# Kernel optimization log

Measured on AMD Instinct MI355X. Metric: run time of the kernel, lower is better.

## Reference

```python
import jax, jax.numpy as jnp
import numpy as np

N_NODES = 50000
N_EDGES = 800000
F = 64
R = 32


def setup_inputs() -> dict:
    key = jax.random.key(0)
    ks = jax.random.split(key, 12)
    s = jax.random.normal(ks[0], (N_NODES, F), dtype=jnp.float32)
    v = jax.random.normal(ks[1], (N_NODES, 3, F), dtype=jnp.float32)
    radial_embeddings = jax.random.normal(ks[2], (N_EDGES, R), dtype=jnp.float32)
    f_cut = jax.random.uniform(ks[3], (N_EDGES,), dtype=jnp.float32)
    unit_vectors = jax.random.normal(ks[4], (N_EDGES, 3), dtype=jnp.float32)
    edge_index = jax.random.randint(ks[5], (2, N_EDGES), 0, N_NODES, dtype=jnp.int64 if jax.config.jax_enable_x64 else jnp.int32)
    # mlp_phi: Linear(F,F) -> SiLU -> Linear(F, 3F); linear_W: Linear(R, 3F)
    W1 = jax.random.normal(ks[6], (F, F), dtype=jnp.float32) / np.sqrt(F)
    b1 = jnp.zeros((F,), dtype=jnp.float32)
    W2 = jax.random.normal(ks[7], (F, 3 * F), dtype=jnp.float32) / np.sqrt(F)
    b2 = jnp.zeros((3 * F,), dtype=jnp.float32)
    Wr = jax.random.normal(ks[8], (R, 3 * F), dtype=jnp.float32) / np.sqrt(R)
    br = jnp.zeros((3 * F,), dtype=jnp.float32)
    return {"s": s, "v": v, "radial_embeddings": radial_embeddings, "f_cut": f_cut,
            "unit_vectors": unit_vectors, "edge_index": edge_index,
            "W1": W1, "b1": b1, "W2": W2, "b2": b2, "Wr": Wr, "br": br}


def reference(s, v, radial_embeddings, f_cut, unit_vectors, edge_index, W1, b1, W2, b2, Wr, br):
    idx_i, idx_j = edge_index[0], edge_index[1]
    n_nodes = s.shape[0]
    nf = s.shape[-1]
    # per-node MLP: Linear -> SiLU -> Linear to 3F channels
    phi = jax.nn.silu(s @ W1 + b1) @ W2 + b2            # [N, 3F]
    # radial filter weighted by cutoff
    W = (radial_embeddings @ Wr + br) * f_cut[:, None]   # [E, 3F]
    x = phi[idx_j] * W                                   # [E, 3F]  (gather + multiply)
    x_s, x_vv, x_vs = x[:, :nf], x[:, nf:2 * nf], x[:, 2 * nf:]
    ds = jax.ops.segment_sum(x_s, idx_i, num_segments=n_nodes)          # [N, F]
    x_v = v[idx_j] * x_vv[:, None, :] + x_vs[:, None, :] * unit_vectors[:, :, None]  # [E, 3, F]
    dv = jax.ops.segment_sum(x_v, idx_i, num_segments=n_nodes)          # [N, 3, F]
    return s + ds, v + dv
```

## Files before the change

### kernel.cpp

```cpp
#include <hip/hip_runtime.h>
#include <math.h>

#define N_NODES 50000
#define N_EDGES 800000
#define F 64
#define R 32
#define C3F 192
#define CAP 48
#define MLP_BLOCKS ((N_NODES + 31) / 32)
#define FILL_BLOCKS ((N_EDGES + 255) / 256)

#define REP32(X) X(0) X(1) X(2) X(3) X(4) X(5) X(6) X(7) \
                 X(8) X(9) X(10) X(11) X(12) X(13) X(14) X(15) \
                 X(16) X(17) X(18) X(19) X(20) X(21) X(22) X(23) \
                 X(24) X(25) X(26) X(27) X(28) X(29) X(30) X(31)

__global__ __launch_bounds__(256) void mlp_fill_kernel(
    const float* __restrict__ s, const float* __restrict__ W1,
    const float* __restrict__ b1, const float* __restrict__ W2,
    const float* __restrict__ b2, float* __restrict__ phi,
    const int* __restrict__ eidx, int* __restrict__ counts,
    int2* __restrict__ bucket)
{
    __shared__ float hid_s[32][68];

    if (blockIdx.x >= MLP_BLOCKS) {
        int e = (blockIdx.x - MLP_BLOCKS) * 256 + threadIdx.x;
        if (e < N_EDGES) {
            int i = eidx[e];
            int j = eidx[N_EDGES + e];
            int pos = atomicAdd(&counts[i], 1);
            if (pos < CAP) bucket[(size_t)i * CAP + pos] = make_int2(e, j);
        }
        return;
    }

    int n = threadIdx.x >> 3;
    int seg = threadIdx.x & 7;
    int node = blockIdx.x * 32 + n;
    bool live = node < N_NODES;

    if (live) {
        float sv[F];
        const float4* srow = (const float4*)(s + (size_t)node * F);
#pragma unroll
        for (int q = 0; q < F / 4; q++) {
            float4 t = srow[q];
            sv[4*q+0] = t.x; sv[4*q+1] = t.y; sv[4*q+2] = t.z; sv[4*q+3] = t.w;
        }
        float acc[8];
#pragma unroll
        for (int q = 0; q < 8; q++) acc[q] = b1[seg * 8 + q];
#pragma unroll
        for (int k = 0; k < F; k++) {
            float sk = sv[k];
            const float4* w = (const float4*)(W1 + (size_t)k * F + seg * 8);
            float4 w0 = w[0], w1 = w[1];
            acc[0] += sk * w0.x; acc[1] += sk * w0.y;
            acc[2] += sk * w0.z; acc[3] += sk * w0.w;
            acc[4] += sk * w1.x; acc[5] += sk * w1.y;
            acc[6] += sk * w1.z; acc[7] += sk * w1.w;
        }
#pragma unroll
        for (int q = 0; q < 8; q++) {
            float a = acc[q];
            hid_s[n][seg * 8 + q] = a / (1.f + __expf(-a));
        }
    }
    __syncthreads();

    if (!live) return;

    float hv[F];
#pragma unroll
    for (int q = 0; q < F; q++) hv[q] = hid_s[n][q];

    float acc[24];
#pragma unroll
    for (int q = 0; q < 24; q++) acc[q] = b2[seg * 24 + q];
#pragma unroll
    for (int k = 0; k < F; k++) {
        float hk = hv[k];
        const float4* w = (const float4*)(W2 + (size_t)k * C3F + seg * 24);
#pragma unroll
        for (int q4 = 0; q4 < 6; q4++) {
            float4 wv = w[q4];
            acc[q4*4+0] += hk * wv.x;
            acc[q4*4+1] += hk * wv.y;
            acc[q4*4+2] += hk * wv.z;
            acc[q4*4+3] += hk * wv.w;
        }
    }
    float4* o = (float4*)(phi + (size_t)node * C3F + seg * 24);
#pragma unroll
    for (int q4 = 0; q4 < 6; q4++)
        o[q4] = make_float4(acc[q4*4+0], acc[q4*4+1], acc[q4*4+2], acc[q4*4+3]);
}

__global__ __launch_bounds__(256, 3) void gather_kernel(
    const float* __restrict__ s, const float* __restrict__ v,
    const float* __restrict__ phi, const float* __restrict__ radial,
    const float* __restrict__ f_cut, const float* __restrict__ unit_vec,
    const float* __restrict__ Wr, const float* __restrict__ br,
    const int* __restrict__ counts, const int2* __restrict__ bucket,
    float* __restrict__ out_s, float* __restrict__ out_v)
{
    int lane = threadIdx.x & 63;
    int node = __builtin_amdgcn_readfirstlane(
        (int)blockIdx.x * 4 + (int)(threadIdx.x >> 6));
    if (node >= N_NODES) return;

#define DECL_WR(r) float wrs##r, wrv##r, wrq##r;
    REP32(DECL_WR)
#undef DECL_WR
#define LOAD_WR(r) { const float* w_ = Wr + (r) * C3F; \
                     wrs##r = w_[lane]; wrv##r = w_[64 + lane]; \
                     wrq##r = w_[128 + lane]; }
    REP32(LOAD_WR)
#undef LOAD_WR

    float b_s = br[lane], b_vv = br[64 + lane], b_vs = br[128 + lane];

    float acc_s = 0.f, acc_v0 = 0.f, acc_v1 = 0.f, acc_v2 = 0.f;

    int cnt = __builtin_amdgcn_readfirstlane(counts[node]);
    cnt = cnt < CAP ? cnt : CAP;
    const int2* row = bucket + (size_t)node * CAP;

    if (cnt > 0) {
        int2 ej0 = row[0];
        int e = __builtin_amdgcn_readfirstlane(ej0.x);
        int j = __builtin_amdgcn_readfirstlane(ej0.y);
        const float* pj = phi + (size_t)j * C3F;
        const float* vj = v + (size_t)j * C3F;
        float ps = pj[lane], pvv = pj[64 + lane], pvs = pj[128 + lane];
        float va = vj[lane], vb = vj[64 + lane], vc = vj[128 + lane];

        for (int k = 0; k < cnt; k++) {
            float fc = f_cut[e];
            float u0 = unit_vec[e * 3 + 0];
            float u1 = unit_vec[e * 3 + 1];
            float u2 = unit_vec[e * 3 + 2];
            const float* rp = radial + (size_t)e * R;

            int e_n = e, j_n = j;
            if (k + 1 < cnt) {
                int2 ejn = row[k + 1];
                e_n = __builtin_amdgcn_readfirstlane(ejn.x);
                j_n = __builtin_amdgcn_readfirstlane(ejn.y);
            }
            const float* pn = phi + (size_t)j_n * C3F;
            const float* vn = v + (size_t)j_n * C3F;
            float nps = pn[lane], npvv = pn[64 + lane], npvs = pn[128 + lane];
            float nva = vn[lane], nvb = vn[64 + lane], nvc = vn[128 + lane];

            float ws = b_s, wvv = b_vv, wvs = b_vs;
#define FMA_WR(r) { float rr = rp[r]; ws += rr * wrs##r; \
                    wvv += rr * wrv##r; wvs += rr * wrq##r; }
            REP32(FMA_WR)
#undef FMA_WR

            float xs  = ps  * ws  * fc;
            float xvv = pvv * wvv * fc;
            float xvs = pvs * wvs * fc;
            acc_s  += xs;
            acc_v0 += va * xvv + xvs * u0;
            acc_v1 += vb * xvv + xvs * u1;
            acc_v2 += vc * xvv + xvs * u2;

            e = e_n; j = j_n;
            ps = nps; pvv = npvv; pvs = npvs;
            va = nva; vb = nvb; vc = nvc;
        }
    }

    out_s[(size_t)node * F + lane] = s[(size_t)node * F + lane] + acc_s;
    const float* vi = v + (size_t)node * C3F;
    float* ovi = out_v + (size_t)node * C3F;
    ovi[lane]       = vi[lane]       + acc_v0;
    ovi[64 + lane]  = vi[64 + lane]  + acc_v1;
    ovi[128 + lane] = vi[128 + lane] + acc_v2;
}

extern "C" void kernel_launch(void* const* d_in, const int* in_sizes, int n_in,
                              void* d_out, int out_size, void* d_ws, size_t ws_size,
                              hipStream_t stream)
{
    const float* s      = (const float*)d_in[0];
    const float* v      = (const float*)d_in[1];
    const float* radial = (const float*)d_in[2];
    const float* f_cut  = (const float*)d_in[3];
    const float* unit   = (const float*)d_in[4];
    const int*   eidx   = (const int*)  d_in[5];
    const float* W1     = (const float*)d_in[6];
    const float* b1     = (const float*)d_in[7];
    const float* W2     = (const float*)d_in[8];
    const float* b2     = (const float*)d_in[9];
    const float* Wr     = (const float*)d_in[10];
    const float* br     = (const float*)d_in[11];

    float* out   = (float*)d_out;
    float* out_s = out;
    float* out_v = out + (size_t)N_NODES * F;

    float* phi    = (float*)d_ws;
    int*   counts = (int*)(phi + (size_t)N_NODES * C3F);
    int2*  bucket = (int2*)(counts + N_NODES);

    hipMemsetAsync(counts, 0, N_NODES * sizeof(int), stream);

    mlp_fill_kernel<<<MLP_BLOCKS + FILL_BLOCKS, 256, 0, stream>>>(
        s, W1, b1, W2, b2, phi, eidx, counts, bucket);

    gather_kernel<<<(N_NODES + 3) / 4, 256, 0, stream>>>(
        s, v, phi, radial, f_cut, unit, Wr, br,
        counts, bucket, out_s, out_v);
}
```

Measured before the change: 602.2 us.

## Batch edge metadata loads per wave, pad atomic counters, one-wave gather blocks

The fill pass now handles four edges per thread and pads the per-node counters to 16 ints so atomics on neighbouring nodes do not share cache lines. The gather kernel runs one 64-lane block per node and loads the bucket row, f_cut and unit vectors for all of the node's edges in a single wave-wide load. Each lane loads one radial element, and the values are broadcast with readlane instead of issuing scalar loads per edge. Wr registers are pinned with empty asm, and nontemporal loads and stores are used for streamed data. The padded counters raise the memset size and memory footprint, and the smaller blocks may change occupancy.

```diff
diff --git a/kernel.cpp b/kernel.cpp
--- a/kernel.cpp
+++ b/kernel.cpp
@@ -7,13 +7,19 @@
 #define R 32
 #define C3F 192
 #define CAP 48
+#define CSTRIDE 16
 #define MLP_BLOCKS ((N_NODES + 31) / 32)
-#define FILL_BLOCKS ((N_EDGES + 255) / 256)
+#define FILL_BLOCKS ((N_EDGES + 1023) / 1024)
 
 #define REP32(X) X(0) X(1) X(2) X(3) X(4) X(5) X(6) X(7) \
                  X(8) X(9) X(10) X(11) X(12) X(13) X(14) X(15) \
                  X(16) X(17) X(18) X(19) X(20) X(21) X(22) X(23) \
                  X(24) X(25) X(26) X(27) X(28) X(29) X(30) X(31)
+
+__device__ __forceinline__ float bcastf(float x, int l) {
+    return __uint_as_float((unsigned)__builtin_amdgcn_readlane(
+        (int)__float_as_uint(x), l));
+}
 
 __global__ __launch_bounds__(256) void mlp_fill_kernel(
     const float* __restrict__ s, const float* __restrict__ W1,
@@ -25,12 +31,25 @@
     __shared__ float hid_s[32][68];
 
     if (blockIdx.x >= MLP_BLOCKS) {
-        int e = (blockIdx.x - MLP_BLOCKS) * 256 + threadIdx.x;
-        if (e < N_EDGES) {
-            int i = eidx[e];
-            int j = eidx[N_EDGES + e];
-            int pos = atomicAdd(&counts[i], 1);
-            if (pos < CAP) bucket[(size_t)i * CAP + pos] = make_int2(e, j);
+        int base = (blockIdx.x - MLP_BLOCKS) * 1024 + threadIdx.x;
+        int ii[4], jj[4];
+#pragma unroll
+        for (int q = 0; q < 4; q++) {
+            int e = base + q * 256;
+            ii[q] = -1;
+            if (e < N_EDGES) {
+                ii[q] = __builtin_nontemporal_load(&eidx[e]);
+                jj[q] = __builtin_nontemporal_load(&eidx[N_EDGES + e]);
+            }
+        }
+#pragma unroll
+        for (int q = 0; q < 4; q++) {
+            int e = base + q * 256;
+            if (ii[q] >= 0) {
+                int pos = atomicAdd(&counts[ii[q] * CSTRIDE], 1);
+                if (pos < CAP)
+                    bucket[(size_t)ii[q] * CAP + pos] = make_int2(e, jj[q]);
+            }
         }
         return;
     }
@@ -97,7 +116,7 @@
         o[q4] = make_float4(acc[q4*4+0], acc[q4*4+1], acc[q4*4+2], acc[q4*4+3]);
 }
 
-__global__ __launch_bounds__(256, 3) void gather_kernel(
+__global__ __launch_bounds__(64, 3) void gather_kernel(
     const float* __restrict__ s, const float* __restrict__ v,
     const float* __restrict__ phi, const float* __restrict__ radial,
     const float* __restrict__ f_cut, const float* __restrict__ unit_vec,
@@ -105,10 +124,8 @@
     const int* __restrict__ counts, const int2* __restrict__ bucket,
     float* __restrict__ out_s, float* __restrict__ out_v)
 {
-    int lane = threadIdx.x & 63;
-    int node = __builtin_amdgcn_readfirstlane(
-        (int)blockIdx.x * 4 + (int)(threadIdx.x >> 6));
-    if (node >= N_NODES) return;
+    const int lane = threadIdx.x;
+    const int node = blockIdx.x;
 
 #define DECL_WR(r) float wrs##r, wrv##r, wrq##r;
     REP32(DECL_WR)
@@ -119,43 +136,62 @@
     REP32(LOAD_WR)
 #undef LOAD_WR
 
-    float b_s = br[lane], b_vv = br[64 + lane], b_vs = br[128 + lane];
+#define KA3(r) , "+v"(wrs##r), "+v"(wrv##r), "+v"(wrq##r)
+#define PIN_WR \
+    asm volatile("" : "+v"(wrs0) KA3(1) KA3(2) KA3(3) KA3(4) KA3(5) KA3(6) KA3(7), "+v"(wrv0), "+v"(wrq0)); \
+    asm volatile("" : "+v"(wrs8) KA3(9) KA3(10) KA3(11) KA3(12) KA3(13) KA3(14) KA3(15), "+v"(wrv8), "+v"(wrq8)); \
+    asm volatile("" : "+v"(wrs16) KA3(17) KA3(18) KA3(19) KA3(20) KA3(21) KA3(22) KA3(23), "+v"(wrv16), "+v"(wrq16)); \
+    asm volatile("" : "+v"(wrs24) KA3(25) KA3(26) KA3(27) KA3(28) KA3(29) KA3(30) KA3(31), "+v"(wrv24), "+v"(wrq24));
+    PIN_WR
+
+    const float b_s = br[lane], b_vv = br[64 + lane], b_vs = br[128 + lane];
 
     float acc_s = 0.f, acc_v0 = 0.f, acc_v1 = 0.f, acc_v2 = 0.f;
 
-    int cnt = __builtin_amdgcn_readfirstlane(counts[node]);
+    int cnt = __builtin_amdgcn_readfirstlane(counts[node * CSTRIDE]);
     cnt = cnt < CAP ? cnt : CAP;
-    const int2* row = bucket + (size_t)node * CAP;
+
+    const int* rowi = (const int*)(bucket + (size_t)node * CAP);
+    int ejx = 0, ejy = 0;
+    if (lane < cnt) {
+        ejx = __builtin_nontemporal_load(rowi + 2 * lane);
+        ejy = __builtin_nontemporal_load(rowi + 2 * lane + 1);
+    }
+    float fcL = __builtin_nontemporal_load(&f_cut[ejx]);
+    float u0L = __builtin_nontemporal_load(&unit_vec[ejx * 3 + 0]);
+    float u1L = __builtin_nontemporal_load(&unit_vec[ejx * 3 + 1]);
+    float u2L = __builtin_nontemporal_load(&unit_vec[ejx * 3 + 2]);
 
     if (cnt > 0) {
-        int2 ej0 = row[0];
-        int e = __builtin_amdgcn_readfirstlane(ej0.x);
-        int j = __builtin_amdgcn_readfirstlane(ej0.y);
+        int e = __builtin_amdgcn_readlane(ejx, 0);
+        int j = __builtin_amdgcn_readlane(ejy, 0);
         const float* pj = phi + (size_t)j * C3F;
         const float* vj = v + (size_t)j * C3F;
         float ps = pj[lane], pvv = pj[64 + lane], pvs = pj[128 + lane];
         float va = vj[lane], vb = vj[64 + lane], vc = vj[128 + lane];
-
-        for (int k = 0; k < cnt; k++) {
-            float fc = f_cut[e];
-            float u0 = unit_vec[e * 3 + 0];
-            float u1 = unit_vec[e * 3 + 1];
-            float u2 = unit_vec[e * 3 + 2];
-            const float* rp = radial + (size_t)e * R;
-
-            int e_n = e, j_n = j;
-            if (k + 1 < cnt) {
-                int2 ejn = row[k + 1];
-                e_n = __builtin_amdgcn_readfirstlane(ejn.x);
-                j_n = __builtin_amdgcn_readfirstlane(ejn.y);
-            }
-            const float* pn = phi + (size_t)j_n * C3F;
-            const float* vn = v + (size_t)j_n * C3F;
+        float rl = __builtin_nontemporal_load(
+            &radial[(size_t)(unsigned)e * R + (lane & 31)]);
+
+        for (int k = 0; k < cnt; ++k) {
+            int kn = (k + 1 < cnt) ? k + 1 : k;
+            int j_n = __builtin_amdgcn_readlane(ejy, kn);
+            int e_n = __builtin_amdgcn_readlane(ejx, kn);
+            const float* pn = phi + (size_t)(unsigned)j_n * C3F;
+            const float* vn = v + (size_t)(unsigned)j_n * C3F;
             float nps = pn[lane], npvv = pn[64 + lane], npvs = pn[128 + lane];
             float nva = vn[lane], nvb = vn[64 + lane], nvc = vn[128 + lane];
+            float nrl = __builtin_nontemporal_load(
+                &radial[(size_t)(unsigned)e_n * R + (lane & 31)]);
+
+            float fc = bcastf(fcL, k);
+            float u0 = bcastf(u0L, k);
+            float u1 = bcastf(u1L, k);
+            float u2 = bcastf(u2L, k);
+
+            PIN_WR
 
             float ws = b_s, wvv = b_vv, wvs = b_vs;
-#define FMA_WR(r) { float rr = rp[r]; ws += rr * wrs##r; \
+#define FMA_WR(r) { float rr = bcastf(rl, r); ws += rr * wrs##r; \
                     wvv += rr * wrv##r; wvs += rr * wrq##r; }
             REP32(FMA_WR)
 #undef FMA_WR
@@ -171,15 +207,19 @@
             e = e_n; j = j_n;
             ps = nps; pvv = npvv; pvs = npvs;
             va = nva; vb = nvb; vc = nvc;
-        }
-    }
-
-    out_s[(size_t)node * F + lane] = s[(size_t)node * F + lane] + acc_s;
+            rl = nrl;
+        }
+    }
+#undef KA3
+#undef PIN_WR
+
+    float so = s[(size_t)node * F + lane] + acc_s;
+    __builtin_nontemporal_store(so, &out_s[(size_t)node * F + lane]);
     const float* vi = v + (size_t)node * C3F;
     float* ovi = out_v + (size_t)node * C3F;
-    ovi[lane]       = vi[lane]       + acc_v0;
-    ovi[64 + lane]  = vi[64 + lane]  + acc_v1;
-    ovi[128 + lane] = vi[128 + lane] + acc_v2;
+    __builtin_nontemporal_store(vi[lane]       + acc_v0, &ovi[lane]);
+    __builtin_nontemporal_store(vi[64 + lane]  + acc_v1, &ovi[64 + lane]);
+    __builtin_nontemporal_store(vi[128 + lane] + acc_v2, &ovi[128 + lane]);
 }
 
 extern "C" void kernel_launch(void* const* d_in, const int* in_sizes, int n_in,
@@ -205,14 +245,14 @@
 
     float* phi    = (float*)d_ws;
     int*   counts = (int*)(phi + (size_t)N_NODES * C3F);
-    int2*  bucket = (int2*)(counts + N_NODES);
-
-    hipMemsetAsync(counts, 0, N_NODES * sizeof(int), stream);
+    int2*  bucket = (int2*)(counts + (size_t)N_NODES * CSTRIDE);
+
+    hipMemsetAsync(counts, 0, (size_t)N_NODES * CSTRIDE * sizeof(int), stream);
 
     mlp_fill_kernel<<<MLP_BLOCKS + FILL_BLOCKS, 256, 0, stream>>>(
         s, W1, b1, W2, b2, phi, eidx, counts, bucket);
 
-    gather_kernel<<<(N_NODES + 3) / 4, 256, 0, stream>>>(
+    gather_kernel<<<N_NODES, 64, 0, stream>>>(
         s, v, phi, radial, f_cut, unit, Wr, br,
         counts, bucket, out_s, out_v);
 }
```

Result: no change. 605.5 us (+0.6%).
